# Performance work log

Hardware: AMD Instinct MI355X
Metric: run time of the kernel (lower is better)

## Reference

```python
import jax, jax.numpy as jnp
import numpy as np

N = 9            # digits
NC = N * N       # 81 cells
H = 128          # hidden1
B = 2048         # batch of puzzles


def _constraint_mask():
    idx = np.arange(NC)
    r, c = idx // N, idx % N
    cm = np.zeros((3, NC, NC), np.float32)
    cm[0] = (r[:, None] == r[None, :])
    cm[1] = (c[:, None] == c[None, :])
    cm[2] = ((r[:, None] // 3 == r[None, :] // 3) & (c[:, None] // 3 == c[None, :] // 3))
    return cm


def setup_inputs() -> dict:
    key = jax.random.key(0)
    k1, k2, k3, k4 = jax.random.split(key, 4)
    digits = jax.random.randint(k1, (B, NC), 0, N)
    given = (jax.random.uniform(k2, (B, NC)) < 0.45).astype(jnp.float32)
    x = jax.nn.one_hot(digits, N, dtype=jnp.float32) * given[:, :, None]
    W1 = jax.random.normal(k3, (H, 3 * N), jnp.float32) * 0.05  # torch Linear weight [out,in]
    W2 = jax.random.normal(k4, (N, H), jnp.float32) * 0.05
    return {"x": x, "W1": W1, "W2": W2,
            "constraint_mask": jnp.asarray(_constraint_mask())}


def reference(x, W1, W2, constraint_mask):
    bts = x.shape[0]
    bidx = jnp.arange(bts)

    def step(carry, _):
        xc, x_pred = carry
        # constraints[b,r,q,e] = sum_k cm[r,q,k] * x[b,k,e]   (same math as
        # (x.unsqueeze(1).unsqueeze(1) * c).sum(dim=3), without the 5D temp)
        cons = jnp.einsum('rqk,bke->brqe', constraint_mask, xc)
        f = cons.reshape(bts, NC, 3 * N)          # matches torch row-major reshape
        empty = (xc.sum(-1) == 0)                 # [b,81] empty-cell mask
        h = jax.nn.relu(f @ W1.T)                 # [b,81,H]
        y = h @ W2.T                              # [b,81,9]
        s_full = jax.nn.softmax(y, axis=-1)       # softmax over digit dim
        x_pred = jnp.where(empty[:, :, None], s_full, x_pred)
        s = jnp.where(empty[:, :, None], s_full, 0.0)
        score = s.max(-1)                         # [b,81]
        pos = s.argmax(-1)                        # [b,81] best digit per cell
        mmax = score.argmax(-1)                   # [b] most confident cell
        has_empty = empty.any(-1)                 # [b] boards with work left
        digit = pos[bidx, mmax]                   # [b]
        upd = (jax.nn.one_hot(mmax, NC, dtype=xc.dtype)[:, :, None]
               * jax.nn.one_hot(digit, N, dtype=xc.dtype)[:, None, :])
        upd = upd * has_empty[:, None, None].astype(xc.dtype)
        xc = jnp.where(upd > 0, jnp.asarray(1.0, xc.dtype), xc)  # index_put_ of ones
        return (xc, x_pred), None

    # original loops min_empty (<=81) times; iterations past min_empty are no-ops
    (xf, x_pred), _ = jax.lax.scan(step, (x, x), None, length=NC)
    return x_pred
```

## Files before the change

### kernel.cpp

```cpp
#include <hip/hip_runtime.h>
#include <cstdint>


__device__ __forceinline__ void wave_fence() {
  asm volatile("s_waitcnt lgkmcnt(0)" ::: "memory");
}

__device__ __forceinline__ int dist_row(int i) {
  int r = i / 27;
  int t = i - 27 * r;
  if (r == 0) return t / 3;
  if (r == 1) return 9 + (t % 3);
  return 12 + 3 * (t / 9) + (t % 3);
}

__device__ __forceinline__ unsigned long long shflx64(unsigned long long v, int m) {
  unsigned lo = (unsigned)v, hi = (unsigned)(v >> 32);
  lo = __shfl_xor(lo, m);
  hi = __shfl_xor(hi, m);
  return ((unsigned long long)hi << 32) | lo;
}

__global__ __launch_bounds__(64, 2)
void sudoku_solver(const float* __restrict__ x, const float* __restrict__ W1g,
                   const float* __restrict__ W2g, float* __restrict__ out) {
  __shared__ float W2s[9][132];
  __shared__ float cnt[3][9][12];
  __shared__ float hbuf[3][132];
  __shared__ float sful[21][12];
  __shared__ float rscore[21];
  __shared__ int   rargs[21];
  __shared__ unsigned long long emask[2];
  __shared__ float yscr[32];
  __shared__ float escr[32];
  __shared__ int   digc[81];

  const int lane = threadIdx.x;
  const int b = blockIdx.x;
  const float* xb = x + b * 729;
  float* ob = out + b * 729;

  for (int idx = lane; idx < 1152; idx += 64)
    W2s[idx >> 7][idx & 127] = W2g[idx];

  float w1a[27], w1b[27];
  #pragma unroll
  for (int c = 0; c < 27; ++c) {
    w1a[c] = W1g[lane * 27 + c];
    w1b[c] = W1g[(lane + 64) * 27 + c];
  }

  for (int idx = lane; idx < 3 * 9 * 12; idx += 64)
    ((float*)cnt)[idx] = 0.f;

  int digA = 0, digB = 0;
  {
    float v[9]; int dg = -1;
    #pragma unroll
    for (int e = 0; e < 9; ++e) v[e] = xb[lane * 9 + e];
    #pragma unroll
    for (int e = 0; e < 9; ++e) { if (v[e] > 0.5f) dg = e; ob[lane * 9 + e] = v[e]; }
    digA = dg; digc[lane] = dg;
    if (lane < 17) {
      const int i2 = 64 + lane;
      float w[9]; int dg2 = -1;
      #pragma unroll
      for (int e = 0; e < 9; ++e) w[e] = xb[i2 * 9 + e];
      #pragma unroll
      for (int e = 0; e < 9; ++e) { if (w[e] > 0.5f) dg2 = e; ob[i2 * 9 + e] = w[e]; }
      digB = dg2; digc[i2] = dg2;
    }
  }
  {
    unsigned long long m0 = __ballot(digA < 0);
    unsigned long long m1 = __ballot((lane < 17) && (digB < 0)) & 0x1FFFFull;
    if (lane == 0) { emask[0] = m0; emask[1] = m1; }
  }
  wave_fence();

  if (lane < 27) {
    const int g = lane / 9, gi = lane - 9 * g;
    float c9[9];
    #pragma unroll
    for (int e = 0; e < 9; ++e) c9[e] = 0.f;
    #pragma unroll
    for (int k = 0; k < 9; ++k) {
      int cell;
      if (g == 0)      cell = gi * 9 + k;
      else if (g == 1) cell = k * 9 + gi;
      else             cell = (gi / 3) * 27 + (gi % 3) * 3 + (k / 3) * 9 + (k % 3);
      const int dg = digc[cell];
      #pragma unroll
      for (int e = 0; e < 9; ++e) c9[e] += (dg == e) ? 1.f : 0.f;
    }
    #pragma unroll
    for (int e = 0; e < 9; ++e) cnt[g][gi][e] = c9[e];
  }
  wave_fence();

  auto update_rows = [&](int u0, int u1, int u2) {
    #pragma unroll
    for (int rr = 0; rr < 3; ++rr) {
      const int u = (rr == 0) ? u0 : (rr == 1) ? u1 : u2;
      int g, gia, gib, gic;
      if (u < 9)       { g = 0; gia = gib = gic = u; }
      else if (u < 12) { g = 1; gia = 3 * (u - 9); gib = gia + 1; gic = gia + 2; }
      else             { g = 2; gia = gib = gic = u - 12; }
      const float* f0 = &cnt[g][gia][0];
      const float* f1 = &cnt[g][gib][0];
      const float* f2 = &cnt[g][gic][0];
      float acc0 = 0.f, acc1 = 0.f;
#define DOT9(FP, BASE)                                                          \
      {                                                                         \
        float4 fA = *(const float4*)(FP);                                       \
        float4 fB = *(const float4*)((FP) + 4);                                 \
        float f8 = (FP)[8];                                                     \
        acc0 = fmaf(fA.x, w1a[BASE+0], acc0); acc1 = fmaf(fA.x, w1b[BASE+0], acc1); \
        acc0 = fmaf(fA.y, w1a[BASE+1], acc0); acc1 = fmaf(fA.y, w1b[BASE+1], acc1); \
        acc0 = fmaf(fA.z, w1a[BASE+2], acc0); acc1 = fmaf(fA.z, w1b[BASE+2], acc1); \
        acc0 = fmaf(fA.w, w1a[BASE+3], acc0); acc1 = fmaf(fA.w, w1b[BASE+3], acc1); \
        acc0 = fmaf(fB.x, w1a[BASE+4], acc0); acc1 = fmaf(fB.x, w1b[BASE+4], acc1); \
        acc0 = fmaf(fB.y, w1a[BASE+5], acc0); acc1 = fmaf(fB.y, w1b[BASE+5], acc1); \
        acc0 = fmaf(fB.z, w1a[BASE+6], acc0); acc1 = fmaf(fB.z, w1b[BASE+6], acc1); \
        acc0 = fmaf(fB.w, w1a[BASE+7], acc0); acc1 = fmaf(fB.w, w1b[BASE+7], acc1); \
        acc0 = fmaf(f8,  w1a[BASE+8], acc0);  acc1 = fmaf(f8,  w1b[BASE+8], acc1);  \
      }
      DOT9(f0, 0)
      DOT9(f1, 9)
      DOT9(f2, 18)
#undef DOT9
      hbuf[rr][lane]      = fmaxf(acc0, 0.f);
      hbuf[rr][64 + lane] = fmaxf(acc1, 0.f);
    }
    wave_fence();

    const int rrl = lane / 9, dl = lane - 9 * (lane / 9);
    if (lane < 27) {
      const float4* hp = (const float4*)&hbuf[rrl][0];
      const float4* wp = (const float4*)&W2s[dl][0];
      float acc = 0.f;
      #pragma unroll 8
      for (int k = 0; k < 32; ++k) {
        float4 hh = hp[k], ww = wp[k];
        acc = fmaf(hh.x, ww.x, acc);
        acc = fmaf(hh.y, ww.y, acc);
        acc = fmaf(hh.z, ww.z, acc);
        acc = fmaf(hh.w, ww.w, acc);
      }
      yscr[lane] = acc;
    }
    wave_fence();

    float eval = 0.f;
    if (lane < 27) {
      float ymax = yscr[rrl * 9];
      #pragma unroll
      for (int dd = 1; dd < 9; ++dd) ymax = fmaxf(ymax, yscr[rrl * 9 + dd]);
      eval = expf(yscr[lane] - ymax);
      escr[lane] = eval;
    }
    wave_fence();
    if (lane < 27) {
      float S = escr[rrl * 9];
      #pragma unroll
      for (int dd = 1; dd < 9; ++dd) S += escr[rrl * 9 + dd];
      const float s = eval / S;
      const int u = (rrl == 0) ? u0 : (rrl == 1) ? u1 : u2;
      sful[u][dl] = s;
    }
    wave_fence();
    if (lane < 3) {
      const int u = (lane == 0) ? u0 : (lane == 1) ? u1 : u2;
      float best = sful[u][0]; int ba = 0;
      #pragma unroll
      for (int dd = 1; dd < 9; ++dd) {
        float s = sful[u][dd];
        if (s > best) { best = s; ba = dd; }
      }
      rscore[u] = best; rargs[u] = ba;
    }
    wave_fence();
  };

  #pragma unroll 1
  for (int p = 0; p < 7; ++p) update_rows(3 * p, 3 * p + 1, 3 * p + 2);

  #pragma unroll 1
  for (int step = 0; step < 81; ++step) {
    const unsigned long long mm0 = emask[0], mm1 = emask[1];

    float s1 = ((mm0 >> lane) & 1ull) ? rscore[dist_row(lane)] : 0.f;
    unsigned long long key =
        ((unsigned long long)__float_as_uint(s1) << 32) | (unsigned)(96 - lane);
    if (lane < 17) {
      const int i2 = 64 + lane;
      float s2 = ((mm1 >> lane) & 1ull) ? rscore[dist_row(i2)] : 0.f;
      unsigned long long k2 =
          ((unsigned long long)__float_as_uint(s2) << 32) | (unsigned)(96 - i2);
      if (k2 > key) key = k2;
    }
    #pragma unroll
    for (int off = 32; off > 0; off >>= 1) {
      unsigned long long o = shflx64(key, off);
      if (o > key) key = o;
    }
    if ((unsigned)(key >> 32) == 0u) continue;

    const int mmax = 96 - (int)(key & 0xFFFFFFFFull);
    const int du = dist_row(mmax);
    const int digit = rargs[du];
    const int r = mmax / 9, c = mmax - 9 * r;
    const int bx = 3 * (mmax / 27) + c / 3;

    if (lane < 3) {
      const int gi = (lane == 0) ? r : (lane == 1) ? c : bx;
      cnt[lane][gi][digit] += 1.f;
    } else if (lane == 3) {
      if (mmax < 64) emask[0] = mm0 & ~(1ull << mmax);
      else           emask[1] = mm1 & ~(1ull << (mmax - 64));
    } else if (lane >= 8 && lane < 17) {
      ob[mmax * 9 + (lane - 8)] = sful[du][lane - 8];
    }
    wave_fence();

    update_rows(r, 9 + c / 3, 12 + bx);
  }
}

extern "C" void kernel_launch(void* const* d_in, const int* in_sizes, int n_in,
                              void* d_out, int out_size, void* d_ws, size_t ws_size,
                              hipStream_t stream) {
  const float* x  = (const float*)d_in[0];
  const float* W1 = (const float*)d_in[1];
  const float* W2 = (const float*)d_in[2];
  float* out = (float*)d_out;
  sudoku_solver<<<dim3(2048), dim3(64), 0, stream>>>(x, W1, W2, out);
}
```

Before: 264.1 us.

## Replace LDS scratch reductions with DPP/swizzle cross-lane softmax and argmax

The W2 matvec, softmax and per-row argmax now run on 16-lane groups. Max and sum reductions use DPP and ds_swizzle instead of round trips through shared-memory scratch with several wave fences. The per-step argmax over cells becomes a float max reduction plus ballot and ctz, and the empty-cell masks live in per-lane registers instead of shared memory. The loop now breaks once no empty cells remain. This shortens the serial per-step latency chain, at the cost of more lanes doing masked work and some risk in tie-breaking semantics.

```diff
diff --git a/kernel.cpp b/kernel.cpp
--- a/kernel.cpp
+++ b/kernel.cpp
@@ -4,6 +4,39 @@
 
 __device__ __forceinline__ void wave_fence() {
   asm volatile("s_waitcnt lgkmcnt(0)" ::: "memory");
+}
+
+template <int CTRL>
+__device__ __forceinline__ float dppf(float v) {
+  return __int_as_float(__builtin_amdgcn_update_dpp(
+      0, __float_as_int(v), CTRL, 0xF, 0xF, true));
+}
+template <int IMM>
+__device__ __forceinline__ float swzf(float v) {
+  return __int_as_float(__builtin_amdgcn_ds_swizzle(__float_as_int(v), IMM));
+}
+__device__ __forceinline__ float redmax16(float v) {
+  v = fmaxf(v, dppf<0xB1>(v));
+  v = fmaxf(v, dppf<0x4E>(v));
+  v = fmaxf(v, swzf<0x101F>(v));
+  v = fmaxf(v, dppf<0x128>(v));
+  return v;
+}
+__device__ __forceinline__ float redsum16(float v) {
+  v += dppf<0xB1>(v);
+  v += dppf<0x4E>(v);
+  v += swzf<0x101F>(v);
+  v += dppf<0x128>(v);
+  return v;
+}
+__device__ __forceinline__ float redmax64(float v) {
+  v = fmaxf(v, dppf<0xB1>(v));
+  v = fmaxf(v, dppf<0x4E>(v));
+  v = fmaxf(v, swzf<0x101F>(v));
+  v = fmaxf(v, dppf<0x128>(v));
+  v = fmaxf(v, swzf<0x401F>(v));
+  v = fmaxf(v, __shfl_xor(v, 32));
+  return v;
 }
 
 __device__ __forceinline__ int dist_row(int i) {
@@ -12,13 +45,6 @@
   if (r == 0) return t / 3;
   if (r == 1) return 9 + (t % 3);
   return 12 + 3 * (t / 9) + (t % 3);
-}
-
-__device__ __forceinline__ unsigned long long shflx64(unsigned long long v, int m) {
-  unsigned lo = (unsigned)v, hi = (unsigned)(v >> 32);
-  lo = __shfl_xor(lo, m);
-  hi = __shfl_xor(hi, m);
-  return ((unsigned long long)hi << 32) | lo;
 }
 
 __global__ __launch_bounds__(64, 2)
@@ -30,9 +56,6 @@
   __shared__ float sful[21][12];
   __shared__ float rscore[21];
   __shared__ int   rargs[21];
-  __shared__ unsigned long long emask[2];
-  __shared__ float yscr[32];
-  __shared__ float escr[32];
   __shared__ int   digc[81];
 
   const int lane = threadIdx.x;
@@ -53,14 +76,14 @@
   for (int idx = lane; idx < 3 * 9 * 12; idx += 64)
     ((float*)cnt)[idx] = 0.f;
 
-  int digA = 0, digB = 0;
+  bool eA, eB = false;
   {
     float v[9]; int dg = -1;
     #pragma unroll
     for (int e = 0; e < 9; ++e) v[e] = xb[lane * 9 + e];
     #pragma unroll
     for (int e = 0; e < 9; ++e) { if (v[e] > 0.5f) dg = e; ob[lane * 9 + e] = v[e]; }
-    digA = dg; digc[lane] = dg;
+    eA = (dg < 0); digc[lane] = dg;
     if (lane < 17) {
       const int i2 = 64 + lane;
       float w[9]; int dg2 = -1;
@@ -68,14 +91,11 @@
       for (int e = 0; e < 9; ++e) w[e] = xb[i2 * 9 + e];
       #pragma unroll
       for (int e = 0; e < 9; ++e) { if (w[e] > 0.5f) dg2 = e; ob[i2 * 9 + e] = w[e]; }
-      digB = dg2; digc[i2] = dg2;
-    }
-  }
-  {
-    unsigned long long m0 = __ballot(digA < 0);
-    unsigned long long m1 = __ballot((lane < 17) && (digB < 0)) & 0x1FFFFull;
-    if (lane == 0) { emask[0] = m0; emask[1] = m1; }
-  }
+      eB = (dg2 < 0); digc[i2] = dg2;
+    }
+  }
+  const int distA = dist_row(lane);
+  const int distB = (lane < 17) ? dist_row(64 + lane) : 0;
   wave_fence();
 
   if (lane < 27) {
@@ -97,6 +117,12 @@
     for (int e = 0; e < 9; ++e) cnt[g][gi][e] = c9[e];
   }
   wave_fence();
+
+  const int rr3 = lane >> 4;
+  const int dl  = lane & 15;
+  const bool dval = (rr3 < 3) && (dl < 9);
+  const float* hrow = hbuf[(rr3 < 3) ? rr3 : 0];
+  const float* wrow = W2s[(dl < 9) ? dl : 0];
 
   auto update_rows = [&](int u0, int u1, int u2) {
     #pragma unroll
@@ -134,50 +160,38 @@
     }
     wave_fence();
 
-    const int rrl = lane / 9, dl = lane - 9 * (lane / 9);
-    if (lane < 27) {
-      const float4* hp = (const float4*)&hbuf[rrl][0];
-      const float4* wp = (const float4*)&W2s[dl][0];
-      float acc = 0.f;
-      #pragma unroll 8
-      for (int k = 0; k < 32; ++k) {
-        float4 hh = hp[k], ww = wp[k];
-        acc = fmaf(hh.x, ww.x, acc);
-        acc = fmaf(hh.y, ww.y, acc);
-        acc = fmaf(hh.z, ww.z, acc);
-        acc = fmaf(hh.w, ww.w, acc);
-      }
-      yscr[lane] = acc;
-    }
-    wave_fence();
-
-    float eval = 0.f;
-    if (lane < 27) {
-      float ymax = yscr[rrl * 9];
-      #pragma unroll
-      for (int dd = 1; dd < 9; ++dd) ymax = fmaxf(ymax, yscr[rrl * 9 + dd]);
-      eval = expf(yscr[lane] - ymax);
-      escr[lane] = eval;
-    }
-    wave_fence();
-    if (lane < 27) {
-      float S = escr[rrl * 9];
-      #pragma unroll
-      for (int dd = 1; dd < 9; ++dd) S += escr[rrl * 9 + dd];
-      const float s = eval / S;
-      const int u = (rrl == 0) ? u0 : (rrl == 1) ? u1 : u2;
-      sful[u][dl] = s;
-    }
-    wave_fence();
-    if (lane < 3) {
-      const int u = (lane == 0) ? u0 : (lane == 1) ? u1 : u2;
-      float best = sful[u][0]; int ba = 0;
-      #pragma unroll
-      for (int dd = 1; dd < 9; ++dd) {
-        float s = sful[u][dd];
-        if (s > best) { best = s; ba = dd; }
-      }
-      rscore[u] = best; rargs[u] = ba;
+    float a0 = 0.f, a1 = 0.f, a2 = 0.f, a3 = 0.f;
+    const float4* hp = (const float4*)hrow;
+    const float4* wp = (const float4*)wrow;
+    #pragma unroll
+    for (int k = 0; k < 32; k += 4) {
+      float4 h0 = hp[k],     ww0 = wp[k];
+      float4 h1 = hp[k + 1], ww1 = wp[k + 1];
+      float4 h2 = hp[k + 2], ww2 = wp[k + 2];
+      float4 h3 = hp[k + 3], ww3 = wp[k + 3];
+      a0 = fmaf(h0.x, ww0.x, a0); a0 = fmaf(h0.y, ww0.y, a0);
+      a0 = fmaf(h0.z, ww0.z, a0); a0 = fmaf(h0.w, ww0.w, a0);
+      a1 = fmaf(h1.x, ww1.x, a1); a1 = fmaf(h1.y, ww1.y, a1);
+      a1 = fmaf(h1.z, ww1.z, a1); a1 = fmaf(h1.w, ww1.w, a1);
+      a2 = fmaf(h2.x, ww2.x, a2); a2 = fmaf(h2.y, ww2.y, a2);
+      a2 = fmaf(h2.z, ww2.z, a2); a2 = fmaf(h2.w, ww2.w, a2);
+      a3 = fmaf(h3.x, ww3.x, a3); a3 = fmaf(h3.y, ww3.y, a3);
+      a3 = fmaf(h3.z, ww3.z, a3); a3 = fmaf(h3.w, ww3.w, a3);
+    }
+    float y = (a0 + a1) + (a2 + a3);
+    y = dval ? y : -1e30f;
+    const float ymax = redmax16(y);
+    const float ev = dval ? expf(y - ymax) : 0.f;
+    const float S = redsum16(ev);
+    const float s = ev / S;
+    const float sm = dval ? s : 0.f;
+    const float rmax = redmax16(sm);
+    unsigned long long bm = __ballot(dval && (sm == rmax));
+    const int u = (rr3 == 0) ? u0 : (rr3 == 1) ? u1 : u2;
+    if (dval) sful[u][dl] = s;
+    if (rr3 < 3 && dl == 0) {
+      rscore[u] = rmax;
+      rargs[u] = __builtin_ctz((unsigned)((bm >> (rr3 * 16)) & 0xFFFFull));
     }
     wave_fence();
   };
@@ -187,40 +201,28 @@
 
   #pragma unroll 1
   for (int step = 0; step < 81; ++step) {
-    const unsigned long long mm0 = emask[0], mm1 = emask[1];
-
-    float s1 = ((mm0 >> lane) & 1ull) ? rscore[dist_row(lane)] : 0.f;
-    unsigned long long key =
-        ((unsigned long long)__float_as_uint(s1) << 32) | (unsigned)(96 - lane);
-    if (lane < 17) {
-      const int i2 = 64 + lane;
-      float s2 = ((mm1 >> lane) & 1ull) ? rscore[dist_row(i2)] : 0.f;
-      unsigned long long k2 =
-          ((unsigned long long)__float_as_uint(s2) << 32) | (unsigned)(96 - i2);
-      if (k2 > key) key = k2;
-    }
-    #pragma unroll
-    for (int off = 32; off > 0; off >>= 1) {
-      unsigned long long o = shflx64(key, off);
-      if (o > key) key = o;
-    }
-    if ((unsigned)(key >> 32) == 0u) continue;
-
-    const int mmax = 96 - (int)(key & 0xFFFFFFFFull);
+    const float sA = eA ? rscore[distA] : 0.f;
+    const float sB = (lane < 17 && eB) ? rscore[distB] : 0.f;
+    const float M = redmax64(fmaxf(sA, sB));
+    if (M <= 0.f) break;
+
+    const unsigned long long m0 = __ballot(sA == M);
+    const unsigned long long m1 = __ballot((lane < 17) && (sB == M));
+    const int mmax = m0 ? __builtin_ctzll(m0) : 64 + __builtin_ctzll(m1);
+
     const int du = dist_row(mmax);
+    const int r = mmax / 9, c = mmax - 9 * r;
+    const int bx = (mmax / 27) * 3 + c / 3;
     const int digit = rargs[du];
-    const int r = mmax / 9, c = mmax - 9 * r;
-    const int bx = 3 * (mmax / 27) + c / 3;
 
     if (lane < 3) {
       const int gi = (lane == 0) ? r : (lane == 1) ? c : bx;
       cnt[lane][gi][digit] += 1.f;
-    } else if (lane == 3) {
-      if (mmax < 64) emask[0] = mm0 & ~(1ull << mmax);
-      else           emask[1] = mm1 & ~(1ull << (mmax - 64));
     } else if (lane >= 8 && lane < 17) {
       ob[mmax * 9 + (lane - 8)] = sful[du][lane - 8];
     }
+    if (lane == mmax) eA = false;
+    if (lane + 64 == mmax) eB = false;
     wave_fence();
 
     update_rows(r, 9 + c / 3, 12 + bx);
```

Result: faster. 242.3 us (-8.3%).
